# Optimization experiments

Hardware: AMD Instinct MI355X
Metric: run time of the kernel (lower is better)

Reference implementation:

```python
import jax, jax.numpy as jnp
import numpy as np

B, T, F, H, OUT = 32, 2048, 64, 256, 64
EPS = 1e-3  # Keras LayerNormalization default epsilon


def _gru(x_seq, kernel, rkernel, bias, return_sequences):
    """Keras GRU (reset_after=True). x_seq: [B,T,Fin]; kernel [Fin,3H]; rkernel [H,3H]; bias [2,3H]."""
    h = x_seq.shape[-1]
    Hd = rkernel.shape[0]
    # precompute input projections for all timesteps (one big GEMM)
    xb = jnp.einsum('btf,fg->btg', x_seq, kernel) + bias[0]  # [B,T,3H]

    def step(h_prev, xt):
        inner = h_prev @ rkernel + bias[1]            # [B,3H]
        xz, xr, xh = jnp.split(xt, 3, axis=-1)
        rz, rr, rh = jnp.split(inner, 3, axis=-1)
        z = jax.nn.sigmoid(xz + rz)
        r = jax.nn.sigmoid(xr + rr)
        hh = jnp.tanh(xh + r * rh)
        h_new = z * h_prev + (1.0 - z) * hh
        return h_new, h_new

    h0 = jnp.zeros((x_seq.shape[0], Hd), dtype=x_seq.dtype)
    h_last, seq = jax.lax.scan(step, h0, jnp.swapaxes(xb, 0, 1))  # scan over T
    if return_sequences:
        return jnp.swapaxes(seq, 0, 1)  # [B,T,H]
    return h_last  # [B,H]


def setup_inputs() -> dict:
    key = jax.random.key(0)
    ks = jax.random.split(key, 10)
    s = 0.05
    return {
        'x': jax.random.normal(ks[0], (B, T, F), dtype=jnp.float32),
        'gamma': jnp.ones((F,), jnp.float32),
        'beta': jnp.zeros((F,), jnp.float32),
        'k1': jax.random.normal(ks[1], (F, 3 * H), jnp.float32) * s,
        'rk1': jax.random.normal(ks[2], (H, 3 * H), jnp.float32) * s,
        'b1': jnp.zeros((2, 3 * H), jnp.float32),
        'k2': jax.random.normal(ks[3], (H, 3 * H), jnp.float32) * s,
        'rk2': jax.random.normal(ks[4], (H, 3 * H), jnp.float32) * s,
        'b2': jnp.zeros((2, 3 * H), jnp.float32),
        'wd': jax.random.normal(ks[5], (H, OUT), jnp.float32) * s,
        'bd': jnp.zeros((OUT,), jnp.float32),
    }


def reference(x, gamma, beta, k1, rk1, b1, k2, rk2, b2, wd, bd):
    # LayerNorm over last (feature) axis
    mu = jnp.mean(x, axis=-1, keepdims=True)
    var = jnp.mean(jnp.square(x - mu), axis=-1, keepdims=True)
    xn = (x - mu) * jax.lax.rsqrt(var + EPS) * gamma + beta
    h1 = _gru(xn, k1, rk1, b1, return_sequences=True)   # [B,T,H]
    h2 = _gru(h1, k2, rk2, b2, return_sequences=False)  # [B,H]
    return h2 @ wd + bd  # [B,OUT]
```

## Files before the change

### kernel.cpp

```cpp
#include <hip/hip_runtime.h>

#define B_    32
#define T_    2048
#define F_    64
#define H_    256
#define OUT_  64
#define G3_   768
#define NWG1  16
#define NWG2  16
#define TOTAL_WG (NWG1 + NWG2)
#define WGT   512

#define PBLK   512
#define XN_BYTES (B_ * T_ * F_ * 2)
#define S1_OFF   XN_BYTES
#define S2_OFF   (S1_OFF + 4 * 16 * PBLK * 2)
#define FLAG_OFF (S2_OFF + 2 * 16 * PBLK * 2)
#define PROG_OFF (FLAG_OFF + 2048)

typedef _Float16 half8 __attribute__((ext_vector_type(8)));
typedef _Float16 half4 __attribute__((ext_vector_type(4)));
typedef float    f32x4 __attribute__((ext_vector_type(4)));
typedef unsigned long long u64;

#define LD_A(p)    __hip_atomic_load((p),  __ATOMIC_RELAXED, __HIP_MEMORY_SCOPE_AGENT)
#define ST_A(p, v) __hip_atomic_store((p), (v), __ATOMIC_RELAXED, __HIP_MEMORY_SCOPE_AGENT)

__device__ __forceinline__ float sigf(float x) {
    x = fminf(fmaxf(x, -30.f), 30.f);
    return 1.f / (1.f + __expf(-x));
}
__device__ __forceinline__ float tanhfast(float x) {
    x = fminf(fmaxf(x, -15.f), 15.f);
    float e = __expf(2.f * x);
    return (e - 1.f) / (e + 1.f);
}
__device__ __forceinline__ unsigned short f16b(float f) {
    union { _Float16 h; unsigned short u; } c; c.h = (_Float16)f; return c.u;
}
__device__ __forceinline__ u64 gather4(unsigned short u, int jl) {
    unsigned int p = (unsigned int)__shfl_xor((int)(unsigned int)u, 1);
    unsigned int lo32 = (jl & 1) ? ((p & 0xffffu) | ((unsigned int)u << 16))
                                 : ((unsigned int)u | (p << 16));
    unsigned int q = (unsigned int)__shfl_xor((int)lo32, 2);
    return (jl & 2) ? (((u64)lo32 << 32) | q)
                    : ((u64)lo32 | ((u64)q << 32));
}

__global__ void init_kernel(float* __restrict__ out, const float* __restrict__ bd,
                            _Float16* __restrict__ packs, unsigned int* __restrict__ flg) {
    int t = blockIdx.x * 256 + threadIdx.x;
    if (t < B_ * OUT_) out[t] = bd[t & (OUT_ - 1)];
    if (t < 1024) flg[t] = 0u;
    for (int p = t; p < 6 * 16 * PBLK; p += 4096) packs[p] = (_Float16)0.f;
}

__global__ __launch_bounds__(256) void ln_kernel(const float* __restrict__ x,
                                                 const float* __restrict__ gamma,
                                                 const float* __restrict__ beta,
                                                 _Float16* __restrict__ xn) {
    const int tid = threadIdx.x;
    const int r = tid >> 4, q = tid & 15;
    const size_t row = (size_t)blockIdx.x * 16 + r;
    const int b = (int)(row >> 11);
    const int t = (int)(row & 2047);
    const float4 v  = *(const float4*)(x + row * F_ + q * 4);
    const float4 g  = *(const float4*)(gamma + q * 4);
    const float4 be = *(const float4*)(beta + q * 4);
    float s = v.x + v.y + v.z + v.w;
    s += __shfl_xor(s, 1, 16); s += __shfl_xor(s, 2, 16);
    s += __shfl_xor(s, 4, 16); s += __shfl_xor(s, 8, 16);
    const float mu = s * (1.f / 64.f);
    const float dx = v.x - mu, dy = v.y - mu, dz = v.z - mu, dw = v.w - mu;
    float qq = dx * dx + dy * dy + dz * dz + dw * dw;
    qq += __shfl_xor(qq, 1, 16); qq += __shfl_xor(qq, 2, 16);
    qq += __shfl_xor(qq, 4, 16); qq += __shfl_xor(qq, 8, 16);
    const float rs = rsqrtf(qq * (1.f / 64.f) + 1e-3f);
    half4 o;
    o[0] = (_Float16)(dx * rs * g.x + be.x);
    o[1] = (_Float16)(dy * rs * g.y + be.y);
    o[2] = (_Float16)(dz * rs * g.z + be.z);
    o[3] = (_Float16)(dw * rs * g.w + be.w);
    *(half4*)(xn + ((size_t)t * B_ + b) * F_ + q * 4) = o;
}

__global__ __launch_bounds__(WGT) void gru_main(
    const _Float16* __restrict__ xn,
    const float* __restrict__ k1, const float* __restrict__ rk1,
    const float* __restrict__ b1, const float* __restrict__ k2,
    const float* __restrict__ rk2, const float* __restrict__ b2,
    const float* __restrict__ wd, float* __restrict__ out,
    _Float16* __restrict__ p1, _Float16* __restrict__ p2,
    unsigned int* __restrict__ flags, unsigned int* __restrict__ prog) {
    const int tid  = threadIdx.x;
    const int lane = tid & 63;
    const int wave = tid >> 6;
    const int mt   = wave & 1;
    const int nt   = wave >> 1;
    const int ln   = lane & 15;
    const int quad = lane >> 4;

    __shared__ _Float16 h1s[32][264];
    __shared__ _Float16 h2s[32][264];
    __shared__ float Cs[2][32][52];
    __shared__ float hs[32][16];

    const int  lc    = nt * 16 + ln;
    const bool valid = (lc < 48);
    const int  gate  = lc >> 4;
    const int  hidx  = lc & 15;
    const int  jl    = tid & 15;
    const int  bb    = tid >> 4;
    const int  m     = mt * 16 + ln;

    if (blockIdx.x < NWG1) {
        const int w    = blockIdx.x;
        const int gcol = valid ? (gate * H_ + w * 16 + hidx) : 0;
        half8 fk1[2], frk1[8];
#pragma unroll
        for (int ks = 0; ks < 2; ++ks) {
            half8 f;
#pragma unroll
            for (int j = 0; j < 8; ++j) {
                const float v = k1[(ks * 32 + quad * 8 + j) * G3_ + gcol];
                f[j] = valid ? (_Float16)v : (_Float16)0.f;
            }
            fk1[ks] = f;
        }
#pragma unroll
        for (int ks = 0; ks < 8; ++ks) {
            half8 f;
#pragma unroll
            for (int j = 0; j < 8; ++j) {
                const float v = rk1[(ks * 32 + quad * 8 + j) * G3_ + gcol];
                f[j] = valid ? (_Float16)v : (_Float16)0.f;
            }
            frk1[ks] = f;
        }
        const int gc = w * 16 + jl;
        const float bxz = b1[gc],       bxr = b1[H_ + gc],       bxh = b1[2 * H_ + gc];
        const float bhz = b1[G3_ + gc], bhr = b1[G3_ + H_ + gc], bhh = b1[G3_ + 2 * H_ + gc];
        float h1m = 0.f;

        const int w2  = tid >> 5;
        const int t32 = tid & 31;
        const unsigned* f1p = flags + w2 * 16;
        const unsigned* f2p = prog  + w2 * 16;

        for (int i = 0; i < T_; ++i) {
            f32x4 c0 = {0.f, 0.f, 0.f, 0.f};
            {
                half8 ax0 = *(const half8*)(xn + ((size_t)i * B_ + m) * F_ + quad * 8);
                half8 ax1 = *(const half8*)(xn + ((size_t)i * B_ + m) * F_ + 32 + quad * 8);
                c0 = __builtin_amdgcn_mfma_f32_16x16x32_f16(ax0, fk1[0], c0, 0, 0, 0);
                c0 = __builtin_amdgcn_mfma_f32_16x16x32_f16(ax1, fk1[1], c0, 0, 0, 0);
            }
            {
                const unsigned tgt1 = (unsigned)i;
                const unsigned tgt2 = (i >= 4) ? (unsigned)(i - 3) : 0u;
                while (LD_A(f1p) < tgt1 || LD_A(f2p) < tgt2)
                    __builtin_amdgcn_s_sleep(1);
                const u64* src = (const u64*)(p1 + (((unsigned)(i + 3) & 3u) * 16 + w2) * PBLK);
                u64 q0 = LD_A(src + t32);
                u64 q1 = LD_A(src + 32 + t32);
                u64 q2 = LD_A(src + 64 + t32);
                u64 q3 = LD_A(src + 96 + t32);
                const int b0 = t32 >> 2;
                const int c0f = w2 * 16 + (t32 & 3) * 4;
                *(u64*)(&h1s[b0][c0f])      = q0;
                *(u64*)(&h1s[b0 + 8][c0f])  = q1;
                *(u64*)(&h1s[b0 + 16][c0f]) = q2;
                *(u64*)(&h1s[b0 + 24][c0f]) = q3;
            }
            __syncthreads();

            f32x4 c1 = {0.f, 0.f, 0.f, 0.f};
#pragma unroll
            for (int ks = 0; ks < 8; ++ks) {
                half8 a1 = *(const half8*)(&h1s[m][ks * 32 + quad * 8]);
                c1 = __builtin_amdgcn_mfma_f32_16x16x32_f16(a1, frk1[ks], c1, 0, 0, 0);
            }
            if (valid) {
                const int r0 = mt * 16 + quad * 4;
#pragma unroll
                for (int rr = 0; rr < 4; ++rr) {
                    Cs[0][r0 + rr][lc] = c0[rr];
                    Cs[1][r0 + rr][lc] = c1[rr];
                }
            }
            __syncthreads();

            {
                const float xz = Cs[0][bb][jl]      + bxz;
                const float xr = Cs[0][bb][16 + jl] + bxr;
                const float xh = Cs[0][bb][32 + jl] + bxh;
                const float rz = Cs[1][bb][jl]      + bhz;
                const float rr = Cs[1][bb][16 + jl] + bhr;
                const float rh = Cs[1][bb][32 + jl] + bhh;
                const float z  = sigf(xz + rz);
                const float r  = sigf(xr + rr);
                const float hh = tanhfast(xh + r * rh);
                h1m = z * h1m + (1.f - z) * hh;
                const u64 v1 = gather4(f16b(h1m), jl);
                if ((jl & 3) == 0)
                    ST_A((u64*)(p1 + ((unsigned)(i & 3) * 16 + w) * PBLK + bb * 16 + jl), v1);
                asm volatile("s_waitcnt vmcnt(0)" ::: "memory");
            }
            __syncthreads();
            if (tid == 0) ST_A(&flags[w * 16], (unsigned)(i + 1));
        }
    } else {
        const int w    = blockIdx.x - NWG1;
        const int gcol = valid ? (gate * H_ + w * 16 + hidx) : 0;
        half8 fk2[8], frk2[8];
#pragma unroll
        for (int ks = 0; ks < 8; ++ks) {
            half8 f2, f3;
#pragma unroll
            for (int j = 0; j < 8; ++j) {
                const int k = ks * 32 + quad * 8 + j;
                const float v2 = k2 [k * G3_ + gcol];
                const float v3 = rk2[k * G3_ + gcol];
                f2[j] = valid ? (_Float16)v2 : (_Float16)0.f;
                f3[j] = valid ? (_Float16)v3 : (_Float16)0.f;
            }
            fk2[ks] = f2; frk2[ks] = f3;
        }
        const int gc = w * 16 + jl;
        const float bxz = b2[gc],       bxr = b2[H_ + gc],       bxh = b2[2 * H_ + gc];
        const float bhz = b2[G3_ + gc], bhr = b2[G3_ + H_ + gc], bhh = b2[G3_ + 2 * H_ + gc];
        float h2m = 0.f;

        const int pk  = tid >> 8;
        const int tt  = tid & 255;
        const int w2  = tt >> 4;
        const int l16 = tt & 15;
        const unsigned* fp = pk ? (flags + (16 + w2) * 16) : (flags + w2 * 16);

        for (int t = 0; t < T_; ++t) {
            {
                const unsigned tgt = pk ? (unsigned)t : (unsigned)(t + 1);
                while (LD_A(fp) < tgt) __builtin_amdgcn_s_sleep(1);
                const u64* src = pk
                    ? (const u64*)(p2 + (((unsigned)(t + 1) & 1u) * 16 + w2) * PBLK)
                    : (const u64*)(p1 + (((unsigned)t & 3u) * 16 + w2) * PBLK);
                u64 q[8];
#pragma unroll
                for (int k = 0; k < 8; ++k) q[k] = LD_A(src + k * 16 + l16);
                _Float16 (*dst)[264] = pk ? h2s : h1s;
                const int c0f = w2 * 16 + (l16 & 3) * 4;
                const int b0  = l16 >> 2;
#pragma unroll
                for (int k = 0; k < 8; ++k)
                    *(u64*)(&dst[b0 + k * 4][c0f]) = q[k];
            }
            __syncthreads();
            if (tid == 0) ST_A(&prog[w * 16], (unsigned)(t + 1));

            f32x4 c2 = {0.f, 0.f, 0.f, 0.f};
            f32x4 c3 = c2;
#pragma unroll
            for (int ks = 0; ks < 8; ++ks) {
                half8 a1 = *(const half8*)(&h1s[m][ks * 32 + quad * 8]);
                half8 a2 = *(const half8*)(&h2s[m][ks * 32 + quad * 8]);
                c2 = __builtin_amdgcn_mfma_f32_16x16x32_f16(a1, fk2[ks],  c2, 0, 0, 0);
                c3 = __builtin_amdgcn_mfma_f32_16x16x32_f16(a2, frk2[ks], c3, 0, 0, 0);
            }
            if (valid) {
                const int r0 = mt * 16 + quad * 4;
#pragma unroll
                for (int rr = 0; rr < 4; ++rr) {
                    Cs[0][r0 + rr][lc] = c2[rr];
                    Cs[1][r0 + rr][lc] = c3[rr];
                }
            }
            __syncthreads();

            {
                const float xz = Cs[0][bb][jl]      + bxz;
                const float xr = Cs[0][bb][16 + jl] + bxr;
                const float xh = Cs[0][bb][32 + jl] + bxh;
                const float rz = Cs[1][bb][jl]      + bhz;
                const float rr = Cs[1][bb][16 + jl] + bhr;
                const float rh = Cs[1][bb][32 + jl] + bhh;
                const float z  = sigf(xz + rz);
                const float r  = sigf(xr + rr);
                const float hh = tanhfast(xh + r * rh);
                h2m = z * h2m + (1.f - z) * hh;
                const u64 v2 = gather4(f16b(h2m), jl);
                if ((jl & 3) == 0)
                    ST_A((u64*)(p2 + ((unsigned)(t & 1) * 16 + w) * PBLK + bb * 16 + jl), v2);
                asm volatile("s_waitcnt vmcnt(0)" ::: "memory");
            }
            __syncthreads();
            if (tid == 0) ST_A(&flags[(16 + w) * 16], (unsigned)(t + 1));
        }

        hs[bb][jl] = h2m;
        __syncthreads();
        const int o  = tid & 63;
        const int bq = tid >> 6;
        for (int pass = 0; pass < 4; ++pass) {
            const int b = pass * 8 + bq;
            float acc = 0.f;
#pragma unroll
            for (int j = 0; j < 16; ++j) acc += hs[b][j] * wd[(w * 16 + j) * OUT_ + o];
            atomicAdd(&out[b * OUT_ + o], acc);
        }
    }
}

extern "C" void kernel_launch(void* const* d_in, const int* in_sizes, int n_in,
                              void* d_out, int out_size, void* d_ws, size_t ws_size,
                              hipStream_t stream) {
    const float* x     = (const float*)d_in[0];
    const float* gamma = (const float*)d_in[1];
    const float* beta  = (const float*)d_in[2];
    const float* k1    = (const float*)d_in[3];
    const float* rk1   = (const float*)d_in[4];
    const float* b1    = (const float*)d_in[5];
    const float* k2    = (const float*)d_in[6];
    const float* rk2   = (const float*)d_in[7];
    const float* b2    = (const float*)d_in[8];
    const float* wd    = (const float*)d_in[9];
    const float* bd    = (const float*)d_in[10];
    float* out = (float*)d_out;

    char* ws = (char*)d_ws;
    _Float16*     xn    = (_Float16*)ws;
    _Float16*     p1    = (_Float16*)(ws + S1_OFF);
    _Float16*     p2    = (_Float16*)(ws + S2_OFF);
    unsigned int* flags = (unsigned int*)(ws + FLAG_OFF);
    unsigned int* prog  = (unsigned int*)(ws + PROG_OFF);

    hipLaunchKernelGGL(init_kernel, dim3(16), dim3(256), 0, stream, out, bd, p1, flags);
    hipLaunchKernelGGL(ln_kernel, dim3(B_ * T_ / 16), dim3(256), 0, stream, x, gamma, beta, xn);

    void* args[] = {(void*)&xn, (void*)&k1, (void*)&rk1, (void*)&b1, (void*)&k2,
                    (void*)&rk2, (void*)&b2, (void*)&wd, (void*)&out,
                    (void*)&p1, (void*)&p2, (void*)&flags, (void*)&prog};
    hipLaunchCooperativeKernel((void*)gru_main, dim3(TOTAL_WG), dim3(WGT), args, 0, stream);
}
```

Before: 5.519 ms.

## Halve GRU workgroups per layer and double hidden columns per workgroup

Repartitions the persistent two-layer GRU so each layer runs on 8 workgroups of 1024 threads, each owning 32 hidden units instead of 16. This cuts the number of cross-workgroup flag waits and exchange partners per timestep. The cost is more MFMA and gate work per workgroup on the serial critical path, and 1024-thread blocks that may limit register budget. The layer-1 wait on layer-2 progress is also split out of the combined spin loop.

```diff
diff --git a/kernel.cpp b/kernel.cpp
--- a/kernel.cpp
+++ b/kernel.cpp
@@ -6,17 +6,17 @@
 #define H_    256
 #define OUT_  64
 #define G3_   768
-#define NWG1  16
-#define NWG2  16
+#define NWG1  8
+#define NWG2  8
 #define TOTAL_WG (NWG1 + NWG2)
-#define WGT   512
-
-#define PBLK   512
+#define WGT   1024
+
+#define PBLK   1024
 #define XN_BYTES (B_ * T_ * F_ * 2)
 #define S1_OFF   XN_BYTES
-#define S2_OFF   (S1_OFF + 4 * 16 * PBLK * 2)
-#define FLAG_OFF (S2_OFF + 2 * 16 * PBLK * 2)
-#define PROG_OFF (FLAG_OFF + 2048)
+#define S2_OFF   (S1_OFF + 4 * 8 * PBLK * 2)
+#define FLAG_OFF (S2_OFF + 2 * 8 * PBLK * 2)
+#define PROG_OFF (FLAG_OFF + 1024)
 
 typedef _Float16 half8 __attribute__((ext_vector_type(8)));
 typedef _Float16 half4 __attribute__((ext_vector_type(4)));
@@ -52,7 +52,7 @@
     int t = blockIdx.x * 256 + threadIdx.x;
     if (t < B_ * OUT_) out[t] = bd[t & (OUT_ - 1)];
     if (t < 1024) flg[t] = 0u;
-    for (int p = t; p < 6 * 16 * PBLK; p += 4096) packs[p] = (_Float16)0.f;
+    for (int p = t; p < 6 * 8 * PBLK; p += 4096) packs[p] = (_Float16)0.f;
 }
 
 __global__ __launch_bounds__(256) void ln_kernel(const float* __restrict__ x,
@@ -102,20 +102,20 @@
 
     __shared__ _Float16 h1s[32][264];
     __shared__ _Float16 h2s[32][264];
-    __shared__ float Cs[2][32][52];
-    __shared__ float hs[32][16];
+    __shared__ float Cs[2][32][100];
+    __shared__ float hs[32][32];
 
     const int  lc    = nt * 16 + ln;
-    const bool valid = (lc < 48);
-    const int  gate  = lc >> 4;
-    const int  hidx  = lc & 15;
-    const int  jl    = tid & 15;
-    const int  bb    = tid >> 4;
+    const bool valid = (lc < 96);
+    const int  gate  = lc >> 5;
+    const int  hidx  = lc & 31;
+    const int  jl    = tid & 31;
+    const int  bb    = tid >> 5;
     const int  m     = mt * 16 + ln;
 
     if (blockIdx.x < NWG1) {
         const int w    = blockIdx.x;
-        const int gcol = valid ? (gate * H_ + w * 16 + hidx) : 0;
+        const int gcol = valid ? (gate * H_ + w * 32 + hidx) : 0;
         half8 fk1[2], frk1[8];
 #pragma unroll
         for (int ks = 0; ks < 2; ++ks) {
@@ -137,13 +137,13 @@
             }
             frk1[ks] = f;
         }
-        const int gc = w * 16 + jl;
+        const int gc = w * 32 + jl;
         const float bxz = b1[gc],       bxr = b1[H_ + gc],       bxh = b1[2 * H_ + gc];
         const float bhz = b1[G3_ + gc], bhr = b1[G3_ + H_ + gc], bhh = b1[G3_ + 2 * H_ + gc];
         float h1m = 0.f;
 
-        const int w2  = tid >> 5;
-        const int t32 = tid & 31;
+        const int w2   = tid >> 7;
+        const int t128 = tid & 127;
         const unsigned* f1p = flags + w2 * 16;
         const unsigned* f2p = prog  + w2 * 16;
 
@@ -155,22 +155,20 @@
                 c0 = __builtin_amdgcn_mfma_f32_16x16x32_f16(ax0, fk1[0], c0, 0, 0, 0);
                 c0 = __builtin_amdgcn_mfma_f32_16x16x32_f16(ax1, fk1[1], c0, 0, 0, 0);
             }
+            if (i >= 4) {
+                const unsigned tg2 = (unsigned)(i - 3);
+                while (LD_A(f2p) < tg2) __builtin_amdgcn_s_sleep(1);
+            }
             {
                 const unsigned tgt1 = (unsigned)i;
-                const unsigned tgt2 = (i >= 4) ? (unsigned)(i - 3) : 0u;
-                while (LD_A(f1p) < tgt1 || LD_A(f2p) < tgt2)
-                    __builtin_amdgcn_s_sleep(1);
-                const u64* src = (const u64*)(p1 + (((unsigned)(i + 3) & 3u) * 16 + w2) * PBLK);
-                u64 q0 = LD_A(src + t32);
-                u64 q1 = LD_A(src + 32 + t32);
-                u64 q2 = LD_A(src + 64 + t32);
-                u64 q3 = LD_A(src + 96 + t32);
-                const int b0 = t32 >> 2;
-                const int c0f = w2 * 16 + (t32 & 3) * 4;
-                *(u64*)(&h1s[b0][c0f])      = q0;
-                *(u64*)(&h1s[b0 + 8][c0f])  = q1;
-                *(u64*)(&h1s[b0 + 16][c0f]) = q2;
-                *(u64*)(&h1s[b0 + 24][c0f]) = q3;
+                while (LD_A(f1p) < tgt1) __builtin_amdgcn_s_sleep(1);
+                const u64* src = (const u64*)(p1 + (((unsigned)(i + 3) & 3u) * 8 + w2) * PBLK);
+                u64 q0 = LD_A(src + t128);
+                u64 q1 = LD_A(src + 128 + t128);
+                const int b0 = t128 >> 3;
+                const int cu = t128 & 7;
+                *(u64*)(&h1s[b0][w2 * 32 + cu * 4])      = q0;
+                *(u64*)(&h1s[b0 + 16][w2 * 32 + cu * 4]) = q1;
             }
             __syncthreads();
 
@@ -192,18 +190,18 @@
 
             {
                 const float xz = Cs[0][bb][jl]      + bxz;
-                const float xr = Cs[0][bb][16 + jl] + bxr;
-                const float xh = Cs[0][bb][32 + jl] + bxh;
+                const float xr = Cs[0][bb][32 + jl] + bxr;
+                const float xh = Cs[0][bb][64 + jl] + bxh;
                 const float rz = Cs[1][bb][jl]      + bhz;
-                const float rr = Cs[1][bb][16 + jl] + bhr;
-                const float rh = Cs[1][bb][32 + jl] + bhh;
+                const float rr = Cs[1][bb][32 + jl] + bhr;
+                const float rh = Cs[1][bb][64 + jl] + bhh;
                 const float z  = sigf(xz + rz);
                 const float r  = sigf(xr + rr);
                 const float hh = tanhfast(xh + r * rh);
                 h1m = z * h1m + (1.f - z) * hh;
                 const u64 v1 = gather4(f16b(h1m), jl);
                 if ((jl & 3) == 0)
-                    ST_A((u64*)(p1 + ((unsigned)(i & 3) * 16 + w) * PBLK + bb * 16 + jl), v1);
+                    ST_A((u64*)(p1 + ((unsigned)(i & 3) * 8 + w) * PBLK + bb * 32 + jl), v1);
                 asm volatile("s_waitcnt vmcnt(0)" ::: "memory");
             }
             __syncthreads();
@@ -211,7 +209,7 @@
         }
     } else {
         const int w    = blockIdx.x - NWG1;
-        const int gcol = valid ? (gate * H_ + w * 16 + hidx) : 0;
+        const int gcol = valid ? (gate * H_ + w * 32 + hidx) : 0;
         half8 fk2[8], frk2[8];
 #pragma unroll
         for (int ks = 0; ks < 8; ++ks) {
@@ -226,33 +224,33 @@
             }
             fk2[ks] = f2; frk2[ks] = f3;
         }
-        const int gc = w * 16 + jl;
+        const int gc = w * 32 + jl;
         const float bxz = b2[gc],       bxr = b2[H_ + gc],       bxh = b2[2 * H_ + gc];
         const float bhz = b2[G3_ + gc], bhr = b2[G3_ + H_ + gc], bhh = b2[G3_ + 2 * H_ + gc];
         float h2m = 0.f;
 
-        const int pk  = tid >> 8;
-        const int tt  = tid & 255;
-        const int w2  = tt >> 4;
-        const int l16 = tt & 15;
-        const unsigned* fp = pk ? (flags + (16 + w2) * 16) : (flags + w2 * 16);
+        const int pk  = tid >> 9;
+        const int tt  = tid & 511;
+        const int w2  = tt >> 6;
+        const int l64 = tt & 63;
+        const unsigned* fp = pk ? (flags + (8 + w2) * 16) : (flags + w2 * 16);
 
         for (int t = 0; t < T_; ++t) {
             {
                 const unsigned tgt = pk ? (unsigned)t : (unsigned)(t + 1);
                 while (LD_A(fp) < tgt) __builtin_amdgcn_s_sleep(1);
                 const u64* src = pk
-                    ? (const u64*)(p2 + (((unsigned)(t + 1) & 1u) * 16 + w2) * PBLK)
-                    : (const u64*)(p1 + (((unsigned)t & 3u) * 16 + w2) * PBLK);
-                u64 q[8];
-#pragma unroll
-                for (int k = 0; k < 8; ++k) q[k] = LD_A(src + k * 16 + l16);
+                    ? (const u64*)(p2 + (((unsigned)(t + 1) & 1u) * 8 + w2) * PBLK)
+                    : (const u64*)(p1 + (((unsigned)t & 3u) * 8 + w2) * PBLK);
+                u64 q[4];
+#pragma unroll
+                for (int k = 0; k < 4; ++k) q[k] = LD_A(src + k * 64 + l64);
                 _Float16 (*dst)[264] = pk ? h2s : h1s;
-                const int c0f = w2 * 16 + (l16 & 3) * 4;
-                const int b0  = l16 >> 2;
-#pragma unroll
-                for (int k = 0; k < 8; ++k)
-                    *(u64*)(&dst[b0 + k * 4][c0f]) = q[k];
+#pragma unroll
+                for (int k = 0; k < 4; ++k) {
+                    const int idx = k * 64 + l64;
+                    *(u64*)(&dst[idx >> 3][w2 * 32 + (idx & 7) * 4]) = q[k];
+                }
             }
             __syncthreads();
             if (tid == 0) ST_A(&prog[w * 16], (unsigned)(t + 1));
@@ -278,33 +276,33 @@
 
             {
                 const float xz = Cs[0][bb][jl]      + bxz;
-                const float xr = Cs[0][bb][16 + jl] + bxr;
-                const float xh = Cs[0][bb][32 + jl] + bxh;
+                const float xr = Cs[0][bb][32 + jl] + bxr;
+                const float xh = Cs[0][bb][64 + jl] + bxh;
                 const float rz = Cs[1][bb][jl]      + bhz;
-                const float rr = Cs[1][bb][16 + jl] + bhr;
-                const float rh = Cs[1][bb][32 + jl] + bhh;
+                const float rr = Cs[1][bb][32 + jl] + bhr;
+                const float rh = Cs[1][bb][64 + jl] + bhh;
                 const float z  = sigf(xz + rz);
                 const float r  = sigf(xr + rr);
                 const float hh = tanhfast(xh + r * rh);
                 h2m = z * h2m + (1.f - z) * hh;
                 const u64 v2 = gather4(f16b(h2m), jl);
                 if ((jl & 3) == 0)
-                    ST_A((u64*)(p2 + ((unsigned)(t & 1) * 16 + w) * PBLK + bb * 16 + jl), v2);
+                    ST_A((u64*)(p2 + ((unsigned)(t & 1) * 8 + w) * PBLK + bb * 32 + jl), v2);
                 asm volatile("s_waitcnt vmcnt(0)" ::: "memory");
             }
             __syncthreads();
-            if (tid == 0) ST_A(&flags[(16 + w) * 16], (unsigned)(t + 1));
+            if (tid == 0) ST_A(&flags[(8 + w) * 16], (unsigned)(t + 1));
         }
 
         hs[bb][jl] = h2m;
         __syncthreads();
         const int o  = tid & 63;
         const int bq = tid >> 6;
-        for (int pass = 0; pass < 4; ++pass) {
-            const int b = pass * 8 + bq;
+        for (int pass = 0; pass < 2; ++pass) {
+            const int b = pass * 16 + bq;
             float acc = 0.f;
 #pragma unroll
-            for (int j = 0; j < 16; ++j) acc += hs[b][j] * wd[(w * 16 + j) * OUT_ + o];
+            for (int j = 0; j < 32; ++j) acc += hs[b][j] * wd[(w * 32 + j) * OUT_ + o];
             atomicAdd(&out[b * OUT_ + o], acc);
         }
     }
```

Measured after the change: 7.288 ms. +32.1%, slower.
